# Kernel tuning notes

Measured on AMD Instinct MI355X. Metric: run time of the kernel, lower is better.

Reference implementation:

```python
import jax, jax.numpy as jnp
import numpy as np

B, N, L, D = 4096, 11, 12, 256
ZDIM = 32
LINE_DIM = 64
PAST_DIM = 6 * D - (2 * D + LINE_DIM)  # 960


def _pos_enc(length, d):
    # PositionalAgentEncoding.build_pos_enc
    pos = jnp.arange(length, dtype=jnp.float32)[:, None]
    div = jnp.exp(jnp.arange(0, d, 2, dtype=jnp.float32) * (-np.log(10000.0) / d))
    pe = jnp.zeros((length, d), dtype=jnp.float32)
    pe = pe.at[:, 0::2].set(jnp.sin(pos * div))
    pe = pe.at[:, 1::2].set(jnp.cos(pos * div))
    return pe


def setup_inputs() -> dict:
    key = jax.random.key(0)
    ks = jax.random.split(key, 16)
    s = 0.02
    return {
        "inputs": jax.random.normal(ks[0], (B * N, L, 4), jnp.float32),
        "past_feature": jax.random.normal(ks[1], (B * N, PAST_DIM), jnp.float32),
        "W_in": jax.random.normal(ks[2], (4, D), jnp.float32) * s,
        "b_in": jnp.zeros((D,), jnp.float32),
        "W_pos": jax.random.normal(ks[3], (2 * D, D), jnp.float32) * s,
        "b_pos": jnp.zeros((D,), jnp.float32),
        "W_fc2": jax.random.normal(ks[4], (L * D, D), jnp.float32) * s,
        "b_fc2": jnp.zeros((D,), jnp.float32),
        "W_fc3": jax.random.normal(ks[5], (D + N, D), jnp.float32) * s,
        "b_fc3": jnp.zeros((D,), jnp.float32),
        "W_msg": jax.random.normal(ks[6], (2 * D, D), jnp.float32) * s,
        "b_msg": jnp.zeros((D,), jnp.float32),
        "W_hyp": jax.random.normal(ks[7], (2 * D, D), jnp.float32) * s,
        "b_hyp": jnp.zeros((D,), jnp.float32),
        "W_line": jax.random.normal(ks[8], (D, LINE_DIM), jnp.float32) * s,
        "W_out": jax.random.normal(ks[9], (6 * D, 128), jnp.float32) * s,
        "b_out": jnp.zeros((128,), jnp.float32),
        "W_qz": jax.random.normal(ks[10], (128, 2 * ZDIM), jnp.float32) * s,
        "b_qz": jnp.zeros((2 * ZDIM,), jnp.float32),
        "batch_size": B,
        "agent_num": N,
    }


def reference(inputs, past_feature, W_in, b_in, W_pos, b_pos, W_fc2, b_fc2,
              W_fc3, b_fc3, W_msg, b_msg, W_hyp, b_hyp, W_line,
              W_out, b_out, W_qz, b_qz, batch_size, agent_num):
    BN, length, _ = inputs.shape
    d = W_in.shape[1]
    bsz, n = batch_size, agent_num
    # input_fc + positional encoding (concat=True, dropout=eval identity)
    tf = inputs @ W_in + b_in                                   # [BN, L, D]
    pe = jnp.broadcast_to(_pos_enc(length, d), (BN, length, d))
    tf = jnp.concatenate([tf, pe], axis=-1) @ W_pos + b_pos     # [BN, L, D]
    # input_fc2 over flattened time, then category concat + input_fc3
    ftraj = tf.reshape(bsz, n, length * d) @ W_fc2 + b_fc2      # [B, N, D]
    cat = jnp.broadcast_to(jnp.eye(n, dtype=ftraj.dtype), (bsz, n, n))
    ftraj = jnp.concatenate([ftraj, cat], axis=-1) @ W_fc3 + b_fc3
    # cosine correlation + per-scene adaptive threshold
    q = ftraj / jnp.linalg.norm(ftraj, axis=2, keepdims=True)
    corr = jnp.einsum('bnd,bmd->bnm', q, q)                     # [B, N, N]
    a = corr.min(axis=(1, 2))
    thr = jnp.where(a < 0.4, 0.4,
                    jnp.where((a > 0.4) & (a < 0.6), a + 0.1, a + 0.03))
    corr = jnp.where(corr < thr[:, None, None], 0.0, corr)
    # ordinary MS_HGNN surrogate: one dense message-passing round
    attn = jax.nn.softmax(jnp.einsum('bnd,bmd->bnm', ftraj, ftraj)
                          / jnp.sqrt(jnp.asarray(d, ftraj.dtype)), axis=-1)
    agg = jnp.einsum('bnm,bmd->bnd', attn, ftraj)
    ftraj_inter = jax.nn.relu(jnp.concatenate([ftraj, agg], -1) @ W_msg + b_msg)
    # hyper/clique surrogate: binarized thresholded corr as incidence, degree-normalized
    A = (corr > 0).astype(ftraj.dtype)
    A = A / jnp.maximum(A.sum(-1, keepdims=True), 1.0)
    hag = jnp.einsum('bnm,bmd->bnd', A, ftraj)
    hyp = jax.nn.relu(jnp.concatenate([ftraj, hag], -1) @ W_hyp + b_hyp)
    feat_bs = hyp @ W_line                                      # [B, N, 64]
    final = jnp.concatenate([ftraj, ftraj_inter, feat_bs], -1).reshape(bsz * n, -1)
    h = jnp.concatenate([past_feature, final], axis=-1)         # [BN, 6D]
    h = jax.nn.relu(h @ W_out + b_out)
    return h @ W_qz + b_qz                                      # [BN, 2*zdim]
```

## Files before the change

### kernel.cpp

```cpp
#include <hip/hip_runtime.h>
#include <hip/hip_bf16.h>

#define BB 4096
#define NNA 11
#define BN (BB*NNA)

#define OFF_WEFF   0
#define OFF_BIASL  1024
#define OFF_WBIG   4096
#define OFF_WALL   16640
#define OFF_WG1F   31744
#define OFF_BIASG1 87040
#define OFF_WG2    99712
#define OFF_WQT    198656
#define OFF_P2T    202752
#define OFF_P3T    205824
#define OFF_INTER  1287552

typedef short bh8 __attribute__((ext_vector_type(8)));
typedef float fx4 __attribute__((ext_vector_type(4)));

__device__ __forceinline__ short f2bs(float v) { __hip_bfloat16 h = __float2bfloat16(v); return *(short*)&h; }


__global__ __launch_bounds__(256) void k_p1(const float* W_in, const float* b_in,
                                            const float* W_pos, const float* b_pos,
                                            float* ws) {
  __shared__ float A[16*512];
  __shared__ float red[4*16*64];
  int t = threadIdx.x, cb = blockIdx.x;
  int ks = t >> 6, c = t & 63, col = cb*64 + c;
  float coef = -logf(10000.f) / 256.f;
  for (int i = t; i < 16*512; i += 256) {
    int row = i >> 9, kk = i & 511;
    float v;
    if (row < 4) v = (kk < 256) ? W_in[row*256 + kk] : 0.f;
    else if (kk < 256) v = b_in[kk];
    else {
      int ii = (kk - 256) >> 1;
      float dv = expf(coef * (float)(2*ii));
      float ang = (float)(row - 4) * dv;
      v = (kk & 1) ? cosf(ang) : sinf(ang);
    }
    A[i] = v;
  }
  __syncthreads();
  float acc[16];
  #pragma unroll
  for (int r = 0; r < 16; ++r) acc[r] = 0.f;
  #pragma unroll 4
  for (int j = 0; j < 128; ++j) {
    int jj = ks*128 + j;
    float b = W_pos[(size_t)jj*256 + col];
    #pragma unroll
    for (int r = 0; r < 16; ++r) acc[r] += A[r*512 + jj] * b;
  }
  #pragma unroll
  for (int r = 0; r < 16; ++r) red[(ks*16 + r)*64 + c] = acc[r];
  __syncthreads();
  for (int i = t; i < 16*64; i += 256) {
    int row = i >> 6, cc = i & 63;
    float s = red[row*64+cc] + red[(16+row)*64+cc] + red[(32+row)*64+cc] + red[(48+row)*64+cc];
    int gcol = cb*64 + cc;
    if (row < 4) ws[OFF_WEFF + row*256 + gcol] = s;
    else         ws[OFF_BIASL + (row-4)*256 + gcol] = s + b_pos[gcol];
  }
}

__global__ __launch_bounds__(256) void k_p2(const float* W_fc2, float* ws) {
  __shared__ float A[5*256];
  __shared__ float red[4*5*64];
  int t = threadIdx.x, cb = blockIdx.x, l = blockIdx.y;
  int ks = t >> 6, c = t & 63, col = cb*64 + c;
  for (int i = t; i < 5*256; i += 256) {
    int row = i >> 8, kk = i & 255;
    A[i] = (row < 4) ? ws[OFF_WEFF + row*256 + kk] : ws[OFF_BIASL + l*256 + kk];
  }
  __syncthreads();
  float acc[5] = {0.f, 0.f, 0.f, 0.f, 0.f};
  #pragma unroll 4
  for (int j = 0; j < 64; ++j) {
    int jj = ks*64 + j;
    float b = W_fc2[(size_t)(l*256 + jj)*256 + col];
    #pragma unroll
    for (int r = 0; r < 5; ++r) acc[r] += A[r*256 + jj] * b;
  }
  #pragma unroll
  for (int r = 0; r < 5; ++r) red[(ks*5 + r)*64 + c] = acc[r];
  __syncthreads();
  for (int i = t; i < 5*64; i += 256) {
    int row = i / 64, cc = i % 64;
    float s = red[row*64+cc] + red[(5+row)*64+cc] + red[(10+row)*64+cc] + red[(15+row)*64+cc];
    int gcol = cb*64 + cc;
    if (row < 4) ws[OFF_WBIG + (l*4 + row)*256 + gcol] = s;
    else         ws[OFF_P2T + l*256 + gcol] = s;
  }
}

__global__ __launch_bounds__(256) void k_p3(const float* W_fc3, const float* b_fc2, float* ws) {
  __shared__ float A[7*256];
  __shared__ float red[4*7*64];
  int t = threadIdx.x, cb = blockIdx.x, rg = blockIdx.y;
  int ks = t >> 6, c = t & 63, col = cb*64 + c;
  for (int i = t; i < 7*256; i += 256) {
    int row = i >> 8, kk = i & 255, gr = rg*7 + row;
    float v;
    if (gr < 48) v = ws[OFF_WBIG + gr*256 + kk];
    else {
      v = b_fc2[kk];
      #pragma unroll
      for (int l = 0; l < 12; ++l) v += ws[OFF_P2T + l*256 + kk];
    }
    A[i] = v;
  }
  __syncthreads();
  float acc[7] = {0.f,0.f,0.f,0.f,0.f,0.f,0.f};
  #pragma unroll 4
  for (int j = 0; j < 64; ++j) {
    int jj = ks*64 + j;
    float b = W_fc3[(size_t)jj*256 + col];
    #pragma unroll
    for (int r = 0; r < 7; ++r) acc[r] += A[r*256 + jj] * b;
  }
  #pragma unroll
  for (int r = 0; r < 7; ++r) red[(ks*7 + r)*64 + c] = acc[r];
  __syncthreads();
  for (int i = t; i < 7*64; i += 256) {
    int row = i / 64, cc = i % 64, gr = rg*7 + row;
    float s = red[row*64+cc] + red[(7+row)*64+cc] + red[(14+row)*64+cc] + red[(21+row)*64+cc];
    int gcol = cb*64 + cc;
    if (gr < 48)       ws[OFF_WALL + gr*256 + gcol] = s;
    else if (gr == 48) ws[OFF_P3T + gcol] = s;
  }
}

__device__ __forceinline__ float wg1_elem(int j, int col, const float* W_msg,
                                          const float* W_hyp, const float* W_out) {
  if (col < 256)       return W_msg[j*256 + col];
  else if (col < 512)  return W_msg[(256+j)*256 + (col-256)];
  else if (col < 768)  return W_hyp[j*256 + (col-512)];
  else if (col < 1024) return W_hyp[(256+j)*256 + (col-768)];
  else                 return W_out[(960+j)*128 + (col-1024)];
}

__global__ __launch_bounds__(256) void k_p4(const float* W_msg, const float* b_msg,
                                            const float* W_hyp, const float* b_hyp,
                                            const float* W_out, const float* W_fc3,
                                            const float* b_fc3, float* ws) {
  __shared__ float A[8*256];
  __shared__ float red[4*8*64];
  int t = threadIdx.x, cb = blockIdx.x, rg = blockIdx.y;
  int ks = t >> 6, c = t & 63, col = cb*64 + c;
  for (int i = t; i < 8*256; i += 256) {
    int row = i >> 8, kk = i & 255, gr = rg*8 + row;
    float v;
    if (gr < 48)      v = ws[OFF_WALL + gr*256 + kk];
    else if (gr < 59) v = ws[OFF_P3T + kk] + b_fc3[kk] + W_fc3[(size_t)(256 + gr - 48)*256 + kk];
    else              v = 0.f;
    A[i] = v;
  }
  __syncthreads();
  float acc[8];
  #pragma unroll
  for (int r = 0; r < 8; ++r) acc[r] = 0.f;
  #pragma unroll 4
  for (int j = 0; j < 64; ++j) {
    int jj = ks*64 + j;
    float b = wg1_elem(jj, col, W_msg, W_hyp, W_out);
    #pragma unroll
    for (int r = 0; r < 8; ++r) acc[r] += A[r*256 + jj] * b;
  }
  #pragma unroll
  for (int r = 0; r < 8; ++r) red[(ks*8 + r)*64 + c] = acc[r];
  __syncthreads();
  for (int i = t; i < 8*64; i += 256) {
    int row = i >> 6, cc = i & 63, gr = rg*8 + row;
    float s = red[row*64+cc] + red[(8+row)*64+cc] + red[(16+row)*64+cc] + red[(24+row)*64+cc];
    int gcol = cb*64 + cc;
    if (gr < 48) {
      ws[OFF_WG1F + gr*1152 + gcol] = s;
    } else if (gr < 59) {
      if (gcol < 256) s += b_msg[gcol];
      else if (gcol >= 512 && gcol < 768) s += b_hyp[gcol-512];
      ws[OFF_BIASG1 + (gr-48)*1152 + gcol] = s;
    }
  }
}

__global__ __launch_bounds__(128) void k_p5(const float* W_line, const float* W_out,
                                            const float* W_qz, float* ws) {
  int t = threadIdx.x;
  if (blockIdx.x >= 1536) {
    int i = (blockIdx.x - 1536)*128 + t;
    int n = i >> 7, k = i & 127;
    short* WQs = (short*)(ws + OFF_WQT);
    WQs[n*128 + k] = f2bs(W_qz[k*64 + n]);
    return;
  }
  int c = t, r = blockIdx.x;
  float v;
  if (r < 960)       v = W_out[r*128 + c];
  else if (r < 1216) v = W_out[(r+256)*128 + c];
  else if (r < 1472) {
    int dd = r - 1216;
    float s = 0.f;
    for (int j = 0; j < 64; ++j)
      s += W_line[dd*64 + j] * W_out[(1472+j)*128 + c];
    v = s;
  } else if (r < 1520) {
    v = ws[OFF_WG1F + (r-1472)*1152 + 1024 + c];
  } else v = 0.f;
  short* WTs = (short*)(ws + OFF_WG2);
  WTs[(size_t)c*1536 + r] = f2bs(v);
}

__global__ __launch_bounds__(256, 2) void k_fm(const float* inputs, const float* W_fc3,
                                               const float* b_fc3, float* ws,
                                               __hip_bfloat16* outI, __hip_bfloat16* outH) {
  __shared__ float XT[48*24];
  __shared__ float F[22*260];
  __shared__ float C[2*121];
  __shared__ float MW[4*121];
  int t = threadIdx.x;
  int R0 = blockIdx.x * 22;
  for (int i = t; i < 22*48; i += 256) {
    int r = i / 48, k = i - r*48;
    XT[k*24 + r] = inputs[(size_t)(R0+r)*48 + k];
  }
  for (int i = t; i < 96; i += 256) { int k = i >> 1, r = 22 + (i & 1); XT[k*24+r] = 0.f; }
  __syncthreads();
  {
    int d = t;
    float acc[24];
    float base = ws[OFF_P3T + d] + b_fc3[d];
    #pragma unroll
    for (int r = 0; r < 24; ++r)
      acc[r] = (r < 22) ? (base + W_fc3[(size_t)(256 + (r % 11))*256 + d]) : 0.f;
    for (int k = 0; k < 48; ++k) {
      float w = ws[OFF_WALL + k*256 + d];
      #pragma unroll
      for (int j = 0; j < 6; ++j) {
        float4 xv = *(const float4*)&XT[k*24 + 4*j];
        acc[4*j+0] += xv.x*w; acc[4*j+1] += xv.y*w;
        acc[4*j+2] += xv.z*w; acc[4*j+3] += xv.w*w;
      }
    }
    #pragma unroll
    for (int r = 0; r < 22; ++r) F[r*260 + d] = acc[r];
  }
  __syncthreads();
  int w = t >> 6, lane = t & 63;
  if (w < 2) {
    const float4* F4 = (const float4*)F;
    for (int p = lane; p < 66; p += 64) {
      int n = 0, pp = p;
      while (pp >= 11 - n) { pp -= 11 - n; ++n; }
      int m = n + pp;
      int ra = (w*11 + n) * 65, rb2 = (w*11 + m) * 65;
      float s = 0.f;
      #pragma unroll 4
      for (int j = 0; j < 64; ++j) {
        float4 a = F4[ra + j], b = F4[rb2 + j];
        s += a.x*b.x + a.y*b.y + a.z*b.z + a.w*b.w;
      }
      C[w*121 + n*11 + m] = s;
      C[w*121 + m*11 + n] = s;
    }
  }
  __syncthreads();
  if (w < 2) {
    float* Cw = C + w*121;
    float rn[11];
    #pragma unroll
    for (int n = 0; n < 11; ++n) rn[n] = 1.f / sqrtf(Cw[n*11+n]);
    float a = 1e30f;
    for (int n = 0; n < 11; ++n)
      for (int m = 0; m < 11; ++m)
        a = fminf(a, Cw[n*11+m] * rn[n] * rn[m]);
    float thr = (a < 0.4f) ? 0.4f : (((a > 0.4f) && (a < 0.6f)) ? a + 0.1f : a + 0.03f);
    if (lane < 11) {
      int n = lane;
      float mx = -1e30f;
      #pragma unroll
      for (int m = 0; m < 11; ++m) mx = fmaxf(mx, Cw[n*11+m]);
      mx *= (1.f/16.f);
      float e[11], ssum = 0.f;
      #pragma unroll
      for (int m = 0; m < 11; ++m) { e[m] = expf(Cw[n*11+m]*(1.f/16.f) - mx); ssum += e[m]; }
      float inv = 1.f / ssum;
      #pragma unroll
      for (int m = 0; m < 11; ++m) MW[w*121 + n*11 + m] = e[m]*inv;
      float keep[11], cnt = 0.f;
      #pragma unroll
      for (int m = 0; m < 11; ++m) {
        float q = Cw[n*11+m] * rn[n] * rn[m];
        keep[m] = (q >= thr) ? 1.f : 0.f; cnt += keep[m];
      }
      float sc = 1.f / fmaxf(cnt, 1.f);
      #pragma unroll
      for (int m = 0; m < 11; ++m) MW[(2+w)*121 + n*11 + m] = keep[m]*sc;
    }
  }
  __syncthreads();
  float aT0[24], aB0[24], aT1[24], aB1[24];
  #pragma unroll
  for (int r = 0; r < 24; ++r) {
    if (r < 22) {
      int nb = OFF_BIASG1 + (r % 11)*1152 + t;
      aT0[r] = ws[nb];
      aB0[r] = ws[nb + 256];
      aT1[r] = ws[nb + 512];
      aB1[r] = ws[nb + 768];
    } else { aT0[r]=0.f; aB0[r]=0.f; aT1[r]=0.f; aB1[r]=0.f; }
  }
  for (int k = 0; k < 48; ++k) {
    float wt0 = ws[OFF_WG1F + k*1152 + t];
    float wb0 = ws[OFF_WG1F + k*1152 + t + 256];
    float wt1 = ws[OFF_WG1F + k*1152 + t + 512];
    float wb1 = ws[OFF_WG1F + k*1152 + t + 768];
    #pragma unroll
    for (int j = 0; j < 6; ++j) {
      float4 xv = *(const float4*)&XT[k*24 + 4*j];
      aT0[4*j+0] += xv.x*wt0; aT0[4*j+1] += xv.y*wt0; aT0[4*j+2] += xv.z*wt0; aT0[4*j+3] += xv.w*wt0;
      aB0[4*j+0] += xv.x*wb0; aB0[4*j+1] += xv.y*wb0; aB0[4*j+2] += xv.z*wb0; aB0[4*j+3] += xv.w*wb0;
      aT1[4*j+0] += xv.x*wt1; aT1[4*j+1] += xv.y*wt1; aT1[4*j+2] += xv.z*wt1; aT1[4*j+3] += xv.w*wt1;
      aB1[4*j+0] += xv.x*wb1; aB1[4*j+1] += xv.y*wb1; aB1[4*j+2] += xv.z*wb1; aB1[4*j+3] += xv.w*wb1;
    }
  }
  #pragma unroll
  for (int s = 0; s < 2; ++s)
    #pragma unroll
    for (int n = 0; n < 11; ++n) {
      float v0 = aT0[s*11+n];
      float v1 = aT1[s*11+n];
      #pragma unroll
      for (int m = 0; m < 11; ++m) {
        v0 += MW[s*121 + n*11 + m]       * aB0[s*11+m];
        v1 += MW[(2+s)*121 + n*11 + m]   * aB1[s*11+m];
      }
      outI[(size_t)(R0 + s*11 + n)*256 + t] = __float2bfloat16(fmaxf(v0, 0.f));
      outH[(size_t)(R0 + s*11 + n)*256 + t] = __float2bfloat16(fmaxf(v1, 0.f));
    }
}

#define A_OFF 0
#define BT_OFF 2304
#define HS_OFF 0
#define WQ_OFF 4352
__global__ __launch_bounds__(256) void k_g2(const float* past, const float* inputs,
                                            const float* b_out, const float* b_qz,
                                            const __hip_bfloat16* interI, const __hip_bfloat16* hypI,
                                            float* ws, float* out) {
  __shared__ short LDS[13056];
  int t = threadIdx.x;
  int R0 = blockIdx.x * 32;
  int w = t >> 6, lane = t & 63, quad = lane >> 4, l16 = lane & 15;
  const short* WTs = (const short*)(ws + OFF_WG2);
  const short* WQs = (const short*)(ws + OFF_WQT);
  const short* intS = (const short*)interI;
  const short* hypS = (const short*)hypI;

  fx4 acc[2][2];
  #pragma unroll
  for (int mt = 0; mt < 2; ++mt)
    #pragma unroll
    for (int reg = 0; reg < 4; ++reg) {
      int nidx = (R0 + mt*16 + quad*4 + reg) % 11;
      #pragma unroll
      for (int nt = 0; nt < 2; ++nt) {
        int col = w*32 + nt*16 + l16;
        acc[mt][nt][reg] = b_out[col] + ws[OFF_BIASG1 + nidx*1152 + 1024 + col];
      }
    }

  int ar = t >> 3, ak = (t & 7) * 8;
  int bn = t >> 1, bkh = (t & 1) * 32;
  for (int ch = 0; ch < 24; ++ch) {
    __syncthreads();
    {
      short tmp[8];
      if (ch < 15) {
        const float4* sp = (const float4*)(past + (size_t)(R0+ar)*960 + ch*64 + ak);
        #pragma unroll
        for (int q = 0; q < 2; ++q) {
          float4 v = sp[q];
          tmp[4*q+0]=f2bs(v.x); tmp[4*q+1]=f2bs(v.y); tmp[4*q+2]=f2bs(v.z); tmp[4*q+3]=f2bs(v.w);
        }
        *(bh8*)&LDS[A_OFF + ar*72 + ak] = *(bh8*)&tmp[0];
      } else if (ch < 23) {
        const short* s = ((ch < 19) ? intS : hypS) + (size_t)(R0+ar)*256 + ((ch < 19) ? (ch-15) : (ch-19))*64 + ak;
        *(bh8*)&LDS[A_OFF + ar*72 + ak] = *(const bh8*)&s[0];
      } else {
        if (ak < 48) {
          const float4* sp = (const float4*)(inputs + (size_t)(R0+ar)*48 + ak);
          #pragma unroll
          for (int q = 0; q < 2; ++q) {
            float4 v = sp[q];
            tmp[4*q+0]=f2bs(v.x); tmp[4*q+1]=f2bs(v.y); tmp[4*q+2]=f2bs(v.z); tmp[4*q+3]=f2bs(v.w);
          }
        } else {
          #pragma unroll
          for (int q = 0; q < 8; ++q) tmp[q] = 0;
        }
        *(bh8*)&LDS[A_OFF + ar*72 + ak] = *(bh8*)&tmp[0];
      }
    }
    {
      const short* s = WTs + (size_t)bn*1536 + ch*64 + bkh;
      #pragma unroll
      for (int q = 0; q < 4; ++q)
        *(bh8*)&LDS[BT_OFF + bn*72 + bkh + q*8] = *(const bh8*)&s[q*8];
    }
    __syncthreads();
    #pragma unroll
    for (int ks = 0; ks < 2; ++ks) {
      int kk = ks*32 + quad*8;
      bh8 a[2], b[2];
      #pragma unroll
      for (int mt = 0; mt < 2; ++mt) a[mt] = *(const bh8*)&LDS[A_OFF + (mt*16 + l16)*72 + kk];
      #pragma unroll
      for (int nt = 0; nt < 2; ++nt) b[nt] = *(const bh8*)&LDS[BT_OFF + (w*32 + nt*16 + l16)*72 + kk];
      #pragma unroll
      for (int mt = 0; mt < 2; ++mt)
        #pragma unroll
        for (int nt = 0; nt < 2; ++nt)
          acc[mt][nt] = __builtin_amdgcn_mfma_f32_16x16x32_bf16(a[mt], b[nt], acc[mt][nt], 0, 0, 0);
    }
  }
  __syncthreads();
  #pragma unroll
  for (int mt = 0; mt < 2; ++mt)
    #pragma unroll
    for (int nt = 0; nt < 2; ++nt)
      #pragma unroll
      for (int reg = 0; reg < 4; ++reg)
        LDS[HS_OFF + (mt*16 + quad*4 + reg)*136 + w*32 + nt*16 + l16] = f2bs(fmaxf(acc[mt][nt][reg], 0.f));
  {
    int n = t >> 2, kh = (t & 3) * 32;
    const short* s = WQs + n*128 + kh;
    #pragma unroll
    for (int q = 0; q < 4; ++q)
      *(bh8*)&LDS[WQ_OFF + n*136 + kh + q*8] = *(const bh8*)&s[q*8];
  }
  __syncthreads();
  fx4 acc2[2];
  {
    float bq = b_qz[w*16 + l16];
    #pragma unroll
    for (int mt = 0; mt < 2; ++mt) { acc2[mt][0]=bq; acc2[mt][1]=bq; acc2[mt][2]=bq; acc2[mt][3]=bq; }
  }
  #pragma unroll
  for (int ks = 0; ks < 4; ++ks) {
    int kk = ks*32 + quad*8;
    bh8 bb = *(const bh8*)&LDS[WQ_OFF + (w*16 + l16)*136 + kk];
    #pragma unroll
    for (int mt = 0; mt < 2; ++mt) {
      bh8 aa = *(const bh8*)&LDS[HS_OFF + (mt*16 + l16)*136 + kk];
      acc2[mt] = __builtin_amdgcn_mfma_f32_16x16x32_bf16(aa, bb, acc2[mt], 0, 0, 0);
    }
  }
  #pragma unroll
  for (int mt = 0; mt < 2; ++mt)
    #pragma unroll
    for (int reg = 0; reg < 4; ++reg)
      out[(size_t)(R0 + mt*16 + quad*4 + reg)*64 + w*16 + l16] = acc2[mt][reg];
}

extern "C" void kernel_launch(void* const* d_in, const int* in_sizes, int n_in,
                              void* d_out, int out_size, void* d_ws, size_t ws_size,
                              hipStream_t stream) {
  const float* inputs = (const float*)d_in[0];
  const float* past   = (const float*)d_in[1];
  const float* W_in   = (const float*)d_in[2];
  const float* b_in   = (const float*)d_in[3];
  const float* W_pos  = (const float*)d_in[4];
  const float* b_pos  = (const float*)d_in[5];
  const float* W_fc2  = (const float*)d_in[6];
  const float* b_fc2  = (const float*)d_in[7];
  const float* W_fc3  = (const float*)d_in[8];
  const float* b_fc3  = (const float*)d_in[9];
  const float* W_msg  = (const float*)d_in[10];
  const float* b_msg  = (const float*)d_in[11];
  const float* W_hyp  = (const float*)d_in[12];
  const float* b_hyp  = (const float*)d_in[13];
  const float* W_line = (const float*)d_in[14];
  const float* W_out  = (const float*)d_in[15];
  const float* b_out  = (const float*)d_in[16];
  const float* W_qz   = (const float*)d_in[17];
  const float* b_qz   = (const float*)d_in[18];
  float* ws = (float*)d_ws;
  __hip_bfloat16* interI = (__hip_bfloat16*)(ws + OFF_INTER);
  __hip_bfloat16* hypI   = interI + (size_t)BN*256;
  float* outp   = (float*)d_out;

  hipLaunchKernelGGL(k_p1,  dim3(4),      dim3(256), 0, stream, W_in, b_in, W_pos, b_pos, ws);
  hipLaunchKernelGGL(k_p2,  dim3(4, 12),  dim3(256), 0, stream, W_fc2, ws);
  hipLaunchKernelGGL(k_p3,  dim3(4, 7),   dim3(256), 0, stream, W_fc3, b_fc2, ws);
  hipLaunchKernelGGL(k_p4,  dim3(18, 8),  dim3(256), 0, stream, W_msg, b_msg, W_hyp, b_hyp, W_out, W_fc3, b_fc3, ws);
  hipLaunchKernelGGL(k_p5,  dim3(1600),   dim3(128), 0, stream, W_line, W_out, W_qz, ws);
  hipLaunchKernelGGL(k_fm,  dim3(2048),   dim3(256), 0, stream, inputs, W_fc3, b_fc3, ws, interI, hypI);
  hipLaunchKernelGGL(k_g2,  dim3(1408),   dim3(256), 0, stream, past, inputs, b_out, b_qz,
                     interI, hypI, ws, outp);
}
```

Baseline: 503.4 us.

## Split fused front/mix kernel into separate correlation and mixing kernels

Splits the fused per-scene kernel in two. A new front kernel handles 4 scenes per block, with all four wavefronts computing the feature Gram matrix, the softmax attention weights and the thresholded hypergraph weights, and writes the mixing matrices to global workspace. A second kernel reloads the inputs and those matrices and does the heavy mixing GEMM stage at the old 2-scene granularity. The aim is to stop half the wavefronts idling during the correlation phase and to ease register and LDS pressure in the mixing stage, at the cost of an extra launch, an extra global round-trip for the matrices and the inputs being read twice.

After: 507.2 us. Within noise of the previous version (+0.8%).

```diff
diff --git a/kernel.cpp b/kernel.cpp
--- a/kernel.cpp
+++ b/kernel.cpp
@@ -15,6 +15,7 @@
 #define OFF_WQT    198656
 #define OFF_P2T    202752
 #define OFF_P3T    205824
+#define OFF_MIX    296320
 #define OFF_INTER  1287552
 
 typedef short bh8 __attribute__((ext_vector_type(8)));
@@ -214,43 +215,39 @@
   WTs[(size_t)c*1536 + r] = f2bs(v);
 }
 
-__global__ __launch_bounds__(256, 2) void k_fm(const float* inputs, const float* W_fc3,
-                                               const float* b_fc3, float* ws,
-                                               __hip_bfloat16* outI, __hip_bfloat16* outH) {
-  __shared__ float XT[48*24];
-  __shared__ float F[22*260];
-  __shared__ float C[2*121];
-  __shared__ float MW[4*121];
+__global__ __launch_bounds__(256) void k_front(const float* inputs, const float* W_fc3,
+                                               const float* b_fc3, float* ws) {
+  __shared__ float XT[48*44];
+  __shared__ float F[44*260];
+  __shared__ float C[4*121];
   int t = threadIdx.x;
-  int R0 = blockIdx.x * 22;
-  for (int i = t; i < 22*48; i += 256) {
+  int R0 = blockIdx.x * 44;
+  for (int i = t; i < 44*48; i += 256) {
     int r = i / 48, k = i - r*48;
-    XT[k*24 + r] = inputs[(size_t)(R0+r)*48 + k];
-  }
-  for (int i = t; i < 96; i += 256) { int k = i >> 1, r = 22 + (i & 1); XT[k*24+r] = 0.f; }
+    XT[k*44 + r] = inputs[(size_t)(R0+r)*48 + k];
+  }
   __syncthreads();
   {
     int d = t;
-    float acc[24];
+    float acc[44];
     float base = ws[OFF_P3T + d] + b_fc3[d];
     #pragma unroll
-    for (int r = 0; r < 24; ++r)
-      acc[r] = (r < 22) ? (base + W_fc3[(size_t)(256 + (r % 11))*256 + d]) : 0.f;
+    for (int r = 0; r < 44; ++r) acc[r] = base + W_fc3[(size_t)(256 + (r % 11))*256 + d];
     for (int k = 0; k < 48; ++k) {
       float w = ws[OFF_WALL + k*256 + d];
       #pragma unroll
-      for (int j = 0; j < 6; ++j) {
-        float4 xv = *(const float4*)&XT[k*24 + 4*j];
+      for (int j = 0; j < 11; ++j) {
+        float4 xv = *(const float4*)&XT[k*44 + 4*j];
         acc[4*j+0] += xv.x*w; acc[4*j+1] += xv.y*w;
         acc[4*j+2] += xv.z*w; acc[4*j+3] += xv.w*w;
       }
     }
     #pragma unroll
-    for (int r = 0; r < 22; ++r) F[r*260 + d] = acc[r];
+    for (int r = 0; r < 44; ++r) F[r*260 + d] = acc[r];
   }
   __syncthreads();
   int w = t >> 6, lane = t & 63;
-  if (w < 2) {
+  {
     const float4* F4 = (const float4*)F;
     for (int p = lane; p < 66; p += 64) {
       int n = 0, pp = p;
@@ -268,7 +265,7 @@
     }
   }
   __syncthreads();
-  if (w < 2) {
+  {
     float* Cw = C + w*121;
     float rn[11];
     #pragma unroll
@@ -278,6 +275,8 @@
       for (int m = 0; m < 11; ++m)
         a = fminf(a, Cw[n*11+m] * rn[n] * rn[m]);
     float thr = (a < 0.4f) ? 0.4f : (((a > 0.4f) && (a < 0.6f)) ? a + 0.1f : a + 0.03f);
+    int scene = blockIdx.x*4 + w;
+    float* mixb = ws + OFF_MIX + (size_t)scene*242;
     if (lane < 11) {
       int n = lane;
       float mx = -1e30f;
@@ -289,7 +288,7 @@
       for (int m = 0; m < 11; ++m) { e[m] = expf(Cw[n*11+m]*(1.f/16.f) - mx); ssum += e[m]; }
       float inv = 1.f / ssum;
       #pragma unroll
-      for (int m = 0; m < 11; ++m) MW[w*121 + n*11 + m] = e[m]*inv;
+      for (int m = 0; m < 11; ++m) mixb[n*11+m] = e[m]*inv;
       float keep[11], cnt = 0.f;
       #pragma unroll
       for (int m = 0; m < 11; ++m) {
@@ -298,8 +297,27 @@
       }
       float sc = 1.f / fmaxf(cnt, 1.f);
       #pragma unroll
-      for (int m = 0; m < 11; ++m) MW[(2+w)*121 + n*11 + m] = keep[m]*sc;
-    }
+      for (int m = 0; m < 11; ++m) mixb[121 + n*11 + m] = keep[m]*sc;
+    }
+  }
+}
+
+__global__ __launch_bounds__(256, 2) void k_mix(const float* inputs, float* ws,
+                                             __hip_bfloat16* outI, __hip_bfloat16* outH) {
+  __shared__ float XT[48*24];
+  __shared__ float MW[4*121];
+  int t = threadIdx.x;
+  int s0 = blockIdx.x * 2;
+  int R0 = s0 * 11;
+  for (int i = t; i < 22*48; i += 256) {
+    int r = i / 48, k = i - r*48;
+    XT[k*24 + r] = inputs[(size_t)(R0+r)*48 + k];
+  }
+  for (int i = t; i < 96; i += 256) { int k = i >> 1, r = 22 + (i & 1); XT[k*24+r] = 0.f; }
+  for (int i = t; i < 484; i += 256) {
+    int gy = i / 242, j = i - gy*242;
+    int s = j / 121, jj = j - s*121;
+    MW[(gy*2 + s)*121 + jj] = ws[OFF_MIX + (size_t)(s0+s)*242 + gy*121 + jj];
   }
   __syncthreads();
   float aT0[24], aB0[24], aT1[24], aB1[24];
@@ -498,7 +516,8 @@
   hipLaunchKernelGGL(k_p3,  dim3(4, 7),   dim3(256), 0, stream, W_fc3, b_fc2, ws);
   hipLaunchKernelGGL(k_p4,  dim3(18, 8),  dim3(256), 0, stream, W_msg, b_msg, W_hyp, b_hyp, W_out, W_fc3, b_fc3, ws);
   hipLaunchKernelGGL(k_p5,  dim3(1600),   dim3(128), 0, stream, W_line, W_out, W_qz, ws);
-  hipLaunchKernelGGL(k_fm,  dim3(2048),   dim3(256), 0, stream, inputs, W_fc3, b_fc3, ws, interI, hypI);
+  hipLaunchKernelGGL(k_front, dim3(1024), dim3(256), 0, stream, inputs, W_fc3, b_fc3, ws);
+  hipLaunchKernelGGL(k_mix, dim3(2048),   dim3(256), 0, stream, inputs, ws, interI, hypI);
   hipLaunchKernelGGL(k_g2,  dim3(1408),   dim3(256), 0, stream, past, inputs, b_out, b_qz,
                      interI, hypI, ws, outp);
 }
```
